# Kernel tuning notes

Hardware: AMD Instinct MI355X
Metric: run time of the kernel (lower is better)

Reference implementation:

```python
import jax, jax.numpy as jnp
import numpy as np

NUM_CLASSES = 8
EPS = 1e-4  # variance epsilon from the original module
MARGIN = 1.0  # __init__ arg; unused in the forward math


def setup_inputs() -> dict:
    key = jax.random.key(0)
    kf, kl = jax.random.split(key)
    features = jax.random.normal(kf, (65536, 2, 256), dtype=jnp.float32)
    labels = jax.random.randint(kl, (65536,), 0, NUM_CLASSES)
    return {"features": features, "labels": labels}


def _loss(features, labels):
    B, V, D = features.shape
    # Views of each sample are stacked into the sample's class group
    X = features.reshape(B * V, D)              # [N, D]
    lab = jnp.repeat(labels, V)                 # [N]
    onehot = (lab[:, None] == jnp.arange(NUM_CLASSES)[None, :]).astype(X.dtype)  # [N, C]

    counts = onehot.sum(axis=0)                 # [C] per-class row counts (all > 1 by construction)
    sums = onehot.T @ X                         # [C, D]
    means = sums / counts[:, None]              # [C, D]
    e2 = onehot.T @ (X * X)                     # [C, D] per-class sum of squares
    # unbiased per-feature variance (torch.var default, ddof=1)
    var = (e2 - counts[:, None] * means * means) / (counts[:, None] - 1.0)
    std = jnp.sqrt(var + EPS)
    std_loss = jnp.sum(jnp.mean(jax.nn.relu(1.0 - std), axis=1))  # sum over classes of mean over features

    # Per-class covariance: cov_c = (X_c - mu_c)^T (X_c - mu_c) / (n_c - 1)
    #                             = (sum_c x x^T - n_c mu mu^T) / (n_c - 1)
    S = jnp.einsum('nc,nd,ne->cde', onehot, X, X)  # [C, D, D]
    cov = (S - counts[:, None, None] * means[:, :, None] * means[:, None, :]) / (
        counts[:, None, None] - 1.0)
    diag = jnp.diagonal(cov, axis1=1, axis2=2)      # [C, D]
    offdiag_sq = jnp.sum(cov * cov, axis=(1, 2)) - jnp.sum(diag * diag, axis=1)
    cov_loss = jnp.sum(offdiag_sq / D)

    return std_loss + cov_loss


def reference(features, labels):
    return _loss(features, labels)
```

## Files before the change

kernel.cpp:

```cpp
#include <hip/hip_runtime.h>
#include <stdint.h>


#define NCLS  8
#define D     256
#define CHUNK 512
#define SEG   256
#define EPSF  1e-4f
#define TMAX  264
#define QLEN  16384

typedef __bf16 bf16x8 __attribute__((ext_vector_type(8)));
typedef float  f32x4  __attribute__((ext_vector_type(4)));

__device__ __forceinline__ unsigned short f2bf(float f) {
    unsigned int x = __float_as_uint(f);
    x += 0x7fffu + ((x >> 16) & 1u);
    return (unsigned short)(x >> 16);
}
__device__ __forceinline__ float bf2f(unsigned short u) {
    return __uint_as_float(((unsigned int)u) << 16);
}
__device__ __forceinline__ uint4 pack8(const f32x4& a, const f32x4& b) {
    return make_uint4(
        (unsigned int)f2bf(a[0]) | ((unsigned int)f2bf(a[1]) << 16),
        (unsigned int)f2bf(a[2]) | ((unsigned int)f2bf(a[3]) << 16),
        (unsigned int)f2bf(b[0]) | ((unsigned int)f2bf(b[1]) << 16),
        (unsigned int)f2bf(b[2]) | ((unsigned int)f2bf(b[3]) << 16));
}
__device__ __forceinline__ void st_tile(unsigned char* lds, const uint4* R,
                                        int kblk, int cblkg) {
    #pragma unroll
    for (int cc = 0; cc < 8; ++cc) {
        int wd = cc >> 1;
        int sh = (cc & 1) * 16;
        unsigned int e0 = (((const unsigned int*)&R[0])[wd] >> sh) & 0xffffu;
        unsigned int e1 = (((const unsigned int*)&R[1])[wd] >> sh) & 0xffffu;
        unsigned int e2 = (((const unsigned int*)&R[2])[wd] >> sh) & 0xffffu;
        unsigned int e3 = (((const unsigned int*)&R[3])[wd] >> sh) & 0xffffu;
        int ccol = cblkg * 8 + cc;
        int byt = ccol * 128 + ((kblk * 8) ^ (cc << 4));
        *(uint2*)(lds + byt) = make_uint2(e0 | (e1 << 16), e2 | (e3 << 16));
    }
}

__global__ void k_hist(const int* __restrict__ labels, int nlab, int vfac,
                       int* __restrict__ counts) {
    __shared__ int lc[NCLS];
    int t = threadIdx.x;
    if (t < NCLS) lc[t] = 0;
    __syncthreads();
    for (int i = blockIdx.x * blockDim.x + t; i < nlab; i += gridDim.x * blockDim.x)
        atomicAdd(&lc[labels[i] & 7], vfac);
    __syncthreads();
    if (t < NCLS && lc[t]) atomicAdd(&counts[t], lc[t]);
}

__global__ void k_offsets(const int* __restrict__ counts,
                          int* __restrict__ offsets, int* __restrict__ cursor) {
    if (threadIdx.x == 0) {
        int acc = 0;
        for (int c = 0; c < NCLS; ++c) { offsets[c] = acc; cursor[c] = acc; acc += counts[c]; }
    }
}

__global__ __launch_bounds__(256) void k_idx(
    const int* __restrict__ labels, int nrows, int vfac,
    int* __restrict__ cursor, int* __restrict__ idx)
{
    __shared__ int lcnt[NCLS], lbase[NCLS];
    int t = threadIdx.x;
    int row = blockIdx.x * SEG + t;
    if (t < NCLS) lcnt[t] = 0;
    __syncthreads();
    int c = 0, rk = 0;
    bool ok = (row < nrows);
    if (ok) {
        c = labels[row / vfac] & 7;
        rk = atomicAdd(&lcnt[c], 1);
    }
    __syncthreads();
    if (t < NCLS) lbase[t] = lcnt[t] ? atomicAdd(&cursor[t], lcnt[t]) : 0;
    __syncthreads();
    if (ok) idx[lbase[c] + rk] = row;
}

__global__ __launch_bounds__(256) void k_gram_g(
    const float* __restrict__ X, const int* __restrict__ idx,
    const int* __restrict__ counts, const int* __restrict__ offsets,
    unsigned short* __restrict__ part, float* __restrict__ csums)
{
    __shared__ __align__(16) unsigned char lds[64 * 256 * 2];

    int t = threadIdx.x;
    int lane = t & 63;
    int w = t >> 6;
    int wrow = w >> 1, wcol = w & 1;
    int kblk = t & 15;
    int cblk0 = t >> 4;

    int nch[NCLS], ofch[NCLS];
    int T = 0;
    for (int c = 0; c < NCLS; ++c) {
        int n = counts[c];
        nch[c] = (n + CHUNK - 1) / CHUNK;
        ofch[c] = T;
        T += nch[c];
    }

    const f32x4 zf = {0.f, 0.f, 0.f, 0.f};

    for (int wk = blockIdx.x; wk < 3 * T; wk += gridDim.x) {
        int item = wk / 3;
        int q = wk - item * 3;
        int c = 0;
        while (c < NCLS - 1 && item >= ofch[c + 1]) ++c;
        int chunk = item - ofch[c];
        int base = offsets[c] + chunk * CHUNK;
        int rows = min(CHUNK, counts[c] - chunk * CHUNK);
        int ntiles = (rows + 63) >> 6;

        int colb = (q == 1) ? 128 : 0;
        bool two = (q == 2);
        int bbase = two ? 128 : 0;

        f32x4 acc[4][4];
        #pragma unroll
        for (int i = 0; i < 4; ++i)
            #pragma unroll
            for (int j = 0; j < 4; ++j)
                #pragma unroll
                for (int r = 0; r < 4; ++r) acc[i][j][r] = 0.f;
        float sumv[8];
        #pragma unroll
        for (int e = 0; e < 8; ++e) sumv[e] = 0.f;

        for (int kt = 0; kt < ntiles; ++kt) {
            int rid[4];
            #pragma unroll
            for (int j = 0; j < 4; ++j) {
                int r = kt * 64 + kblk * 4 + j;
                rid[j] = idx[base + min(r, rows - 1)];
            }
            uint4 R0[4];
            #pragma unroll
            for (int j = 0; j < 4; ++j) {
                int r = kt * 64 + kblk * 4 + j;
                const float* rp = X + ((size_t)rid[j] << 8) + colb + cblk0 * 8;
                f32x4 a = *(const f32x4*)rp;
                f32x4 b = *(const f32x4*)(rp + 4);
                if (r >= rows) { a = zf; b = zf; }
                #pragma unroll
                for (int e = 0; e < 4; ++e) { sumv[e] += a[e]; sumv[4 + e] += b[e]; }
                R0[j] = pack8(a, b);
            }
            uint4 R1[4];
            if (two) {
                #pragma unroll
                for (int j = 0; j < 4; ++j) {
                    int r = kt * 64 + kblk * 4 + j;
                    const float* rp = X + ((size_t)rid[j] << 8) + 128 + cblk0 * 8;
                    f32x4 a = *(const f32x4*)rp;
                    f32x4 b = *(const f32x4*)(rp + 4);
                    if (r >= rows) { a = zf; b = zf; }
                    R1[j] = pack8(a, b);
                }
            }
            __syncthreads();
            st_tile(lds, R0, kblk, cblk0);
            if (two) st_tile(lds, R1, kblk, cblk0 + 16);
            __syncthreads();
            #pragma unroll
            for (int ks = 0; ks < 2; ++ks) {
                int kb2 = ks * 64 + ((lane >> 4) << 4);
                int swz = (lane & 7) << 4;
                bf16x8 bfr[4];
                #pragma unroll
                for (int tj = 0; tj < 4; ++tj) {
                    int ccol = bbase + wcol * 64 + tj * 16 + (lane & 15);
                    bfr[tj] = __builtin_bit_cast(bf16x8,
                        *(const uint4*)(lds + ccol * 128 + (kb2 ^ swz)));
                }
                #pragma unroll
                for (int ti = 0; ti < 4; ++ti) {
                    int ccol = wrow * 64 + ti * 16 + (lane & 15);
                    bf16x8 af = __builtin_bit_cast(bf16x8,
                        *(const uint4*)(lds + ccol * 128 + (kb2 ^ swz)));
                    #pragma unroll
                    for (int tj = 0; tj < 4; ++tj)
                        acc[ti][tj] = __builtin_amdgcn_mfma_f32_16x16x32_bf16(
                            af, bfr[tj], acc[ti][tj], 0, 0, 0);
                }
            }
        }

        unsigned short* dst = part + (size_t)wk * QLEN;
        #pragma unroll
        for (int ti = 0; ti < 4; ++ti) {
            int row0 = wrow * 64 + ti * 16 + ((lane >> 4) << 2);
            #pragma unroll
            for (int tj = 0; tj < 4; ++tj) {
                int col = wcol * 64 + tj * 16 + (lane & 15);
                #pragma unroll
                for (int r = 0; r < 4; ++r)
                    dst[(row0 + r) * 128 + col] = f2bf(acc[ti][tj][r]);
            }
        }

        #pragma unroll
        for (int s = 1; s < 16; s <<= 1)
            #pragma unroll
            for (int e = 0; e < 8; ++e)
                sumv[e] += __shfl_xor(sumv[e], s, 64);
        if (q < 2 && (t & 15) == 0) {
            float* cs = csums + (size_t)item * D + colb + cblk0 * 8;
            #pragma unroll
            for (int e = 0; e < 8; ++e) cs[e] = sumv[e];
        }
        __syncthreads();
    }
}

__global__ __launch_bounds__(256) void k_gsum(
    const float* __restrict__ csums, const int* __restrict__ counts,
    float* __restrict__ gsums)
{
    int c = blockIdx.x;
    int i = threadIdx.x;
    int of = 0;
    for (int cc = 0; cc < c; ++cc) of += (counts[cc] + CHUNK - 1) / CHUNK;
    int nc = (counts[c] + CHUNK - 1) / CHUNK;
    float s = 0.f;
    for (int q = 0; q < nc; ++q) s += csums[(size_t)(of + q) * D + i];
    gsums[c * D + i] = s;
}

__global__ __launch_bounds__(256) void k_loss(
    const unsigned short* __restrict__ part, const float* __restrict__ gsums,
    const int* __restrict__ counts, float* __restrict__ out)
{
    __shared__ float red[256];
    int t = threadIdx.x;
    int nch[NCLS], ofch[NCLS];
    int T = 0;
    for (int c = 0; c < NCLS; ++c) {
        int n = counts[c];
        nch[c] = (n + CHUNK - 1) / CHUNK;
        ofch[c] = T;
        T += nch[c];
    }
    float local = 0.f;
    const int total = NCLS * 3 * QLEN;
    for (int idx = blockIdx.x * blockDim.x + t; idx < total; idx += gridDim.x * blockDim.x) {
        int c = idx / (3 * QLEN);
        int rem = idx - c * (3 * QLEN);
        int q = rem >> 14;
        int ij = rem & (QLEN - 1);
        int il = ij >> 7, jl = ij & 127;
        int gi = il + ((q == 1) ? 128 : 0);
        int gj = jl + ((q == 0) ? 0 : 128);
        const unsigned short* p = part + ((size_t)(ofch[c] * 3 + q)) * QLEN + ij;
        float s = 0.f;
        for (int k = 0; k < nch[c]; ++k) s += bf2f(p[(size_t)k * 3 * QLEN]);
        float n  = (float)counts[c];
        float mi = gsums[c * D + gi] / n;
        float mj = gsums[c * D + gj] / n;
        float cov = (s - n * mi * mj) / (n - 1.f);
        float contrib;
        if (q == 2) {
            contrib = 2.f * cov * cov * (1.f / (float)D);
        } else if (il == jl) {
            float sd = sqrtf(cov + EPSF);
            contrib = fmaxf(1.f - sd, 0.f) * (1.f / (float)D);
        } else {
            contrib = cov * cov * (1.f / (float)D);
        }
        local += contrib;
    }
    red[t] = local;
    __syncthreads();
    for (int s = 128; s > 0; s >>= 1) {
        if (t < s) red[t] += red[t + s];
        __syncthreads();
    }
    if (t == 0) atomicAdd(out, red[0]);
}

extern "C" void kernel_launch(void* const* d_in, const int* in_sizes, int n_in,
                              void* d_out, int out_size, void* d_ws, size_t ws_size,
                              hipStream_t stream)
{
    const float* X      = (const float*)d_in[0];
    const int*   labels = (const int*)d_in[1];
    int nfeat = in_sizes[0];
    int nlab  = in_sizes[1];
    int nrows = nfeat / D;
    int vfac  = nrows / nlab;

    char* ws = (char*)d_ws;
    size_t off_idx   = 0;
    size_t sz_idx    = (size_t)nrows * 4;
    size_t off_part  = (off_idx + sz_idx + 255) & ~(size_t)255;
    size_t sz_part   = (size_t)3 * TMAX * QLEN * 2;
    size_t off_cs    = (off_part + sz_part + 255) & ~(size_t)255;
    size_t sz_cs     = (size_t)TMAX * D * 4;
    size_t off_gs    = (off_cs + sz_cs + 255) & ~(size_t)255;
    size_t sz_gs     = (size_t)NCLS * D * 4;
    size_t off_cnt   = (off_gs + sz_gs + 255) & ~(size_t)255;
    size_t off_ofs   = off_cnt + 64;
    size_t off_cur   = off_ofs + 64;

    int*            idx     = (int*)(ws + off_idx);
    unsigned short* part    = (unsigned short*)(ws + off_part);
    float*          csums   = (float*)(ws + off_cs);
    float*          gsums   = (float*)(ws + off_gs);
    int*            counts  = (int*)(ws + off_cnt);
    int*            offsets = (int*)(ws + off_ofs);
    int*            cursor  = (int*)(ws + off_cur);

    hipMemsetAsync(counts, 0, 64, stream);
    hipMemsetAsync(d_out, 0, (size_t)out_size * sizeof(float), stream);

    k_hist<<<64, 256, 0, stream>>>(labels, nlab, vfac, counts);
    k_offsets<<<1, 64, 0, stream>>>(counts, offsets, cursor);
    k_idx<<<(nrows + SEG - 1) / SEG, SEG, 0, stream>>>(labels, nrows, vfac, cursor, idx);
    k_gram_g<<<3 * TMAX, 256, 0, stream>>>(X, idx, counts, offsets, part, csums);
    k_gsum<<<NCLS, 256, 0, stream>>>(csums, counts, gsums);
    k_loss<<<512, 256, 0, stream>>>(part, gsums, counts, (float*)d_out);
}
```

Before: 134.6 us.

## Pre-transpose sorted rows to bf16 and run Gram with per-class split-K partials

Adds a transpose kernel that gathers class-sorted rows, converts them to bf16 in a feature-major per-chunk layout and computes column sums. A new Gram kernel then reads MFMA fragments straight from global memory with no LDS staging, splitting each class's chunks across G groups so the partial buffer shrinks to 8*3*G tiles. The loss kernel reduces over G instead of per-chunk partials. It adds an extra pass writing roughly 64MB of bf16 and depends on workspace size to pick the path, falling back to the old pipeline otherwise; the idx buffer aliases the partial slab, which is only safe because idx is consumed before the Gram kernel writes.

```diff
diff --git a/kernel.cpp b/kernel.cpp
--- a/kernel.cpp
+++ b/kernel.cpp
@@ -7,7 +7,8 @@
 #define CHUNK 512
 #define SEG   256
 #define EPSF  1e-4f
-#define TMAX  264
+#define TCMAX 263
+#define TMAXF 264
 #define QLEN  16384
 
 typedef __bf16 bf16x8 __attribute__((ext_vector_type(8)));
@@ -21,6 +22,242 @@
 __device__ __forceinline__ float bf2f(unsigned short u) {
     return __uint_as_float(((unsigned int)u) << 16);
 }
+
+__global__ void k_hist(const int* __restrict__ labels, int nlab, int vfac,
+                       int* __restrict__ counts) {
+    __shared__ int lc[NCLS];
+    int t = threadIdx.x;
+    if (t < NCLS) lc[t] = 0;
+    __syncthreads();
+    for (int i = blockIdx.x * blockDim.x + t; i < nlab; i += gridDim.x * blockDim.x)
+        atomicAdd(&lc[labels[i] & 7], vfac);
+    __syncthreads();
+    if (t < NCLS && lc[t]) atomicAdd(&counts[t], lc[t]);
+}
+
+__global__ void k_offsets(const int* __restrict__ counts,
+                          int* __restrict__ offsets, int* __restrict__ cursor) {
+    if (threadIdx.x == 0) {
+        int acc = 0;
+        for (int c = 0; c < NCLS; ++c) { offsets[c] = acc; cursor[c] = acc; acc += counts[c]; }
+    }
+}
+
+__global__ __launch_bounds__(256) void k_idx(
+    const int* __restrict__ labels, int nrows, int vfac,
+    int* __restrict__ cursor, int* __restrict__ idx)
+{
+    __shared__ int lcnt[NCLS], lbase[NCLS];
+    int t = threadIdx.x;
+    int row = blockIdx.x * SEG + t;
+    if (t < NCLS) lcnt[t] = 0;
+    __syncthreads();
+    int c = 0, rk = 0;
+    bool ok = (row < nrows);
+    if (ok) {
+        c = labels[row / vfac] & 7;
+        rk = atomicAdd(&lcnt[c], 1);
+    }
+    __syncthreads();
+    if (t < NCLS) lbase[t] = lcnt[t] ? atomicAdd(&cursor[t], lcnt[t]) : 0;
+    __syncthreads();
+    if (ok) idx[lbase[c] + rk] = row;
+}
+
+__global__ __launch_bounds__(512) void k_tr(
+    const float* __restrict__ X, const int* __restrict__ idx,
+    const int* __restrict__ counts, const int* __restrict__ offsets,
+    unsigned short* __restrict__ sortedT, float* __restrict__ csums)
+{
+    int t = threadIdx.x;
+    int fg = t >> 5, rg = t & 31;
+
+    int nch[NCLS], ofch[NCLS];
+    int T = 0;
+    for (int c = 0; c < NCLS; ++c) {
+        nch[c] = (counts[c] + CHUNK - 1) / CHUNK;
+        ofch[c] = T;
+        T += nch[c];
+    }
+    const f32x4 zf = {0.f, 0.f, 0.f, 0.f};
+
+    for (int wk = blockIdx.x; wk < 2 * T; wk += gridDim.x) {
+        int ch = wk >> 1, ph = wk & 1;
+        int c = 0;
+        while (c < NCLS - 1 && ch >= ofch[c + 1]) ++c;
+        int m = ch - ofch[c];
+        int base = offsets[c] + m * CHUNK;
+        int rows = min(CHUNK, counts[c] - m * CHUNK);
+        unsigned short* out = sortedT + ((size_t)ch << 17);
+
+        for (int p = ph * 2; p < ph * 2 + 2; ++p) {
+            float s0 = 0.f, s1 = 0.f, s2 = 0.f, s3 = 0.f;
+            for (int it = 0; it < 4; ++it) {
+                int r0 = it * 128 + rg * 4;
+                f32x4 v[4];
+                #pragma unroll
+                for (int j = 0; j < 4; ++j) {
+                    int r = r0 + j;
+                    int rid = idx[base + min(r, rows - 1)];
+                    f32x4 x = *(const f32x4*)(X + ((size_t)rid << 8) + p * 64 + fg * 4);
+                    if (r >= rows) x = zf;
+                    v[j] = x;
+                }
+                s0 += v[0][0] + v[1][0] + v[2][0] + v[3][0];
+                s1 += v[0][1] + v[1][1] + v[2][1] + v[3][1];
+                s2 += v[0][2] + v[1][2] + v[2][2] + v[3][2];
+                s3 += v[0][3] + v[1][3] + v[2][3] + v[3][3];
+                #pragma unroll
+                for (int e = 0; e < 4; ++e) {
+                    unsigned int b0 = (unsigned int)f2bf(v[0][e]) | ((unsigned int)f2bf(v[1][e]) << 16);
+                    unsigned int b1 = (unsigned int)f2bf(v[2][e]) | ((unsigned int)f2bf(v[3][e]) << 16);
+                    int f = p * 64 + fg * 4 + e;
+                    *(uint2*)(out + (size_t)f * CHUNK + r0) = make_uint2(b0, b1);
+                }
+            }
+            #pragma unroll
+            for (int sh = 1; sh < 32; sh <<= 1) {
+                s0 += __shfl_xor(s0, sh, 64);
+                s1 += __shfl_xor(s1, sh, 64);
+                s2 += __shfl_xor(s2, sh, 64);
+                s3 += __shfl_xor(s3, sh, 64);
+            }
+            if (rg == 0) {
+                f32x4 sv = {s0, s1, s2, s3};
+                *(f32x4*)(csums + (size_t)ch * D + p * 64 + fg * 4) = sv;
+            }
+        }
+    }
+}
+
+__global__ __launch_bounds__(256) void k_gram_s(
+    const unsigned short* __restrict__ sortedT, const int* __restrict__ counts,
+    unsigned short* __restrict__ part, int G)
+{
+    int t = threadIdx.x;
+    int lane = t & 63;
+    int w = t >> 6;
+    int wr = w >> 1, wc = w & 1;
+
+    int wk = blockIdx.x;
+    int c = wk / (3 * G);
+    int rem = wk - c * (3 * G);
+    int q = rem / G;
+    int g = rem - q * G;
+
+    int och = 0;
+    for (int cc = 0; cc < c; ++cc) och += (counts[cc] + CHUNK - 1) / CHUNK;
+    int nchc = (counts[c] + CHUNK - 1) / CHUNK;
+
+    int rowb = (q == 1) ? 128 : 0;
+    int colb = (q == 0) ? 0 : 128;
+    int fr_a = rowb + wr * 64 + (lane & 15);
+    int fr_b = colb + wc * 64 + (lane & 15);
+    int kh = (lane >> 4) * 8;
+
+    f32x4 acc[4][4];
+    #pragma unroll
+    for (int i = 0; i < 4; ++i)
+        #pragma unroll
+        for (int j = 0; j < 4; ++j)
+            #pragma unroll
+            for (int r = 0; r < 4; ++r) acc[i][j][r] = 0.f;
+
+    for (int m = g; m < nchc; m += G) {
+        const unsigned short* cb = sortedT + ((size_t)(och + m) << 17);
+        const unsigned short* pa = cb + (size_t)fr_a * CHUNK + kh;
+        const unsigned short* pb = cb + (size_t)fr_b * CHUNK + kh;
+        for (int ks = 0; ks < CHUNK / 32; ++ks) {
+            int ke = ks * 32;
+            bf16x8 afr[4], bfr[4];
+            #pragma unroll
+            for (int ti = 0; ti < 4; ++ti)
+                afr[ti] = __builtin_bit_cast(bf16x8,
+                    *(const uint4*)(pa + (size_t)ti * 16 * CHUNK + ke));
+            #pragma unroll
+            for (int tj = 0; tj < 4; ++tj)
+                bfr[tj] = __builtin_bit_cast(bf16x8,
+                    *(const uint4*)(pb + (size_t)tj * 16 * CHUNK + ke));
+            #pragma unroll
+            for (int ti = 0; ti < 4; ++ti)
+                #pragma unroll
+                for (int tj = 0; tj < 4; ++tj)
+                    acc[ti][tj] = __builtin_amdgcn_mfma_f32_16x16x32_bf16(
+                        afr[ti], bfr[tj], acc[ti][tj], 0, 0, 0);
+        }
+    }
+
+    unsigned short* dst = part + (size_t)wk * QLEN;
+    #pragma unroll
+    for (int ti = 0; ti < 4; ++ti) {
+        int row0 = wr * 64 + ti * 16 + ((lane >> 4) << 2);
+        #pragma unroll
+        for (int tj = 0; tj < 4; ++tj) {
+            int col = wc * 64 + tj * 16 + (lane & 15);
+            #pragma unroll
+            for (int r = 0; r < 4; ++r)
+                dst[(row0 + r) * 128 + col] = f2bf(acc[ti][tj][r]);
+        }
+    }
+}
+
+__global__ __launch_bounds__(256) void k_gsum(
+    const float* __restrict__ csums, const int* __restrict__ counts,
+    float* __restrict__ gsums)
+{
+    int c = blockIdx.x;
+    int i = threadIdx.x;
+    int of = 0;
+    for (int cc = 0; cc < c; ++cc) of += (counts[cc] + CHUNK - 1) / CHUNK;
+    int nc = (counts[c] + CHUNK - 1) / CHUNK;
+    float s = 0.f;
+    for (int q = 0; q < nc; ++q) s += csums[(size_t)(of + q) * D + i];
+    gsums[c * D + i] = s;
+}
+
+__global__ __launch_bounds__(256) void k_loss_s(
+    const unsigned short* __restrict__ part, const float* __restrict__ gsums,
+    const int* __restrict__ counts, float* __restrict__ out, int G)
+{
+    __shared__ float red[256];
+    int t = threadIdx.x;
+    float local = 0.f;
+    const int total = NCLS * 3 * QLEN;
+    for (int idx = blockIdx.x * blockDim.x + t; idx < total; idx += gridDim.x * blockDim.x) {
+        int c = idx / (3 * QLEN);
+        int rem = idx - c * (3 * QLEN);
+        int q = rem >> 14;
+        int ij = rem & (QLEN - 1);
+        int il = ij >> 7, jl = ij & 127;
+        int gi = il + ((q == 1) ? 128 : 0);
+        int gj = jl + ((q == 0) ? 0 : 128);
+        const unsigned short* p = part + ((size_t)((c * 3 + q) * G)) * QLEN + ij;
+        float s = 0.f;
+        for (int g = 0; g < G; ++g) s += bf2f(p[(size_t)g * QLEN]);
+        float n  = (float)counts[c];
+        float mi = gsums[c * D + gi] / n;
+        float mj = gsums[c * D + gj] / n;
+        float cov = (s - n * mi * mj) / (n - 1.f);
+        float contrib;
+        if (q == 2) {
+            contrib = 2.f * cov * cov * (1.f / (float)D);
+        } else if (il == jl) {
+            float sd = sqrtf(cov + EPSF);
+            contrib = fmaxf(1.f - sd, 0.f) * (1.f / (float)D);
+        } else {
+            contrib = cov * cov * (1.f / (float)D);
+        }
+        local += contrib;
+    }
+    red[t] = local;
+    __syncthreads();
+    for (int s = 128; s > 0; s >>= 1) {
+        if (t < s) red[t] += red[t + s];
+        __syncthreads();
+    }
+    if (t == 0) atomicAdd(out, red[0]);
+}
+
 __device__ __forceinline__ uint4 pack8(const f32x4& a, const f32x4& b) {
     return make_uint4(
         (unsigned int)f2bf(a[0]) | ((unsigned int)f2bf(a[1]) << 16),
@@ -44,54 +281,12 @@
     }
 }
 
-__global__ void k_hist(const int* __restrict__ labels, int nlab, int vfac,
-                       int* __restrict__ counts) {
-    __shared__ int lc[NCLS];
-    int t = threadIdx.x;
-    if (t < NCLS) lc[t] = 0;
-    __syncthreads();
-    for (int i = blockIdx.x * blockDim.x + t; i < nlab; i += gridDim.x * blockDim.x)
-        atomicAdd(&lc[labels[i] & 7], vfac);
-    __syncthreads();
-    if (t < NCLS && lc[t]) atomicAdd(&counts[t], lc[t]);
-}
-
-__global__ void k_offsets(const int* __restrict__ counts,
-                          int* __restrict__ offsets, int* __restrict__ cursor) {
-    if (threadIdx.x == 0) {
-        int acc = 0;
-        for (int c = 0; c < NCLS; ++c) { offsets[c] = acc; cursor[c] = acc; acc += counts[c]; }
-    }
-}
-
-__global__ __launch_bounds__(256) void k_idx(
-    const int* __restrict__ labels, int nrows, int vfac,
-    int* __restrict__ cursor, int* __restrict__ idx)
-{
-    __shared__ int lcnt[NCLS], lbase[NCLS];
-    int t = threadIdx.x;
-    int row = blockIdx.x * SEG + t;
-    if (t < NCLS) lcnt[t] = 0;
-    __syncthreads();
-    int c = 0, rk = 0;
-    bool ok = (row < nrows);
-    if (ok) {
-        c = labels[row / vfac] & 7;
-        rk = atomicAdd(&lcnt[c], 1);
-    }
-    __syncthreads();
-    if (t < NCLS) lbase[t] = lcnt[t] ? atomicAdd(&cursor[t], lcnt[t]) : 0;
-    __syncthreads();
-    if (ok) idx[lbase[c] + rk] = row;
-}
-
-__global__ __launch_bounds__(256) void k_gram_g(
+__global__ __launch_bounds__(256) void k_gram_f(
     const float* __restrict__ X, const int* __restrict__ idx,
     const int* __restrict__ counts, const int* __restrict__ offsets,
     unsigned short* __restrict__ part, float* __restrict__ csums)
 {
     __shared__ __align__(16) unsigned char lds[64 * 256 * 2];
-
     int t = threadIdx.x;
     int lane = t & 63;
     int w = t >> 6;
@@ -102,12 +297,10 @@
     int nch[NCLS], ofch[NCLS];
     int T = 0;
     for (int c = 0; c < NCLS; ++c) {
-        int n = counts[c];
-        nch[c] = (n + CHUNK - 1) / CHUNK;
+        nch[c] = (counts[c] + CHUNK - 1) / CHUNK;
         ofch[c] = T;
         T += nch[c];
     }
-
     const f32x4 zf = {0.f, 0.f, 0.f, 0.f};
 
     for (int wk = blockIdx.x; wk < 3 * T; wk += gridDim.x) {
@@ -120,7 +313,7 @@
         int rows = min(CHUNK, counts[c] - chunk * CHUNK);
         int ntiles = (rows + 63) >> 6;
 
-        int colb = (q == 1) ? 128 : 0;
+        int colbg = (q == 1) ? 128 : 0;
         bool two = (q == 2);
         int bbase = two ? 128 : 0;
 
@@ -146,7 +339,7 @@
             #pragma unroll
             for (int j = 0; j < 4; ++j) {
                 int r = kt * 64 + kblk * 4 + j;
-                const float* rp = X + ((size_t)rid[j] << 8) + colb + cblk0 * 8;
+                const float* rp = X + ((size_t)rid[j] << 8) + colbg + cblk0 * 8;
                 f32x4 a = *(const f32x4*)rp;
                 f32x4 b = *(const f32x4*)(rp + 4);
                 if (r >= rows) { a = zf; b = zf; }
@@ -206,14 +399,13 @@
                     dst[(row0 + r) * 128 + col] = f2bf(acc[ti][tj][r]);
             }
         }
-
         #pragma unroll
         for (int s = 1; s < 16; s <<= 1)
             #pragma unroll
             for (int e = 0; e < 8; ++e)
                 sumv[e] += __shfl_xor(sumv[e], s, 64);
         if (q < 2 && (t & 15) == 0) {
-            float* cs = csums + (size_t)item * D + colb + cblk0 * 8;
+            float* cs = csums + (size_t)item * D + colbg + cblk0 * 8;
             #pragma unroll
             for (int e = 0; e < 8; ++e) cs[e] = sumv[e];
         }
@@ -221,21 +413,7 @@
     }
 }
 
-__global__ __launch_bounds__(256) void k_gsum(
-    const float* __restrict__ csums, const int* __restrict__ counts,
-    float* __restrict__ gsums)
-{
-    int c = blockIdx.x;
-    int i = threadIdx.x;
-    int of = 0;
-    for (int cc = 0; cc < c; ++cc) of += (counts[cc] + CHUNK - 1) / CHUNK;
-    int nc = (counts[c] + CHUNK - 1) / CHUNK;
-    float s = 0.f;
-    for (int q = 0; q < nc; ++q) s += csums[(size_t)(of + q) * D + i];
-    gsums[c * D + i] = s;
-}
-
-__global__ __launch_bounds__(256) void k_loss(
+__global__ __launch_bounds__(256) void k_loss_f(
     const unsigned short* __restrict__ part, const float* __restrict__ gsums,
     const int* __restrict__ counts, float* __restrict__ out)
 {
@@ -244,8 +422,7 @@
     int nch[NCLS], ofch[NCLS];
     int T = 0;
     for (int c = 0; c < NCLS; ++c) {
-        int n = counts[c];
-        nch[c] = (n + CHUNK - 1) / CHUNK;
+        nch[c] = (counts[c] + CHUNK - 1) / CHUNK;
         ofch[c] = T;
         T += nch[c];
     }
@@ -298,33 +475,72 @@
     int vfac  = nrows / nlab;
 
     char* ws = (char*)d_ws;
-    size_t off_idx   = 0;
-    size_t sz_idx    = (size_t)nrows * 4;
-    size_t off_part  = (off_idx + sz_idx + 255) & ~(size_t)255;
-    size_t sz_part   = (size_t)3 * TMAX * QLEN * 2;
-    size_t off_cs    = (off_part + sz_part + 255) & ~(size_t)255;
-    size_t sz_cs     = (size_t)TMAX * D * 4;
-    size_t off_gs    = (off_cs + sz_cs + 255) & ~(size_t)255;
-    size_t sz_gs     = (size_t)NCLS * D * 4;
-    size_t off_cnt   = (off_gs + sz_gs + 255) & ~(size_t)255;
-    size_t off_ofs   = off_cnt + 64;
-    size_t off_cur   = off_ofs + 64;
-
-    int*            idx     = (int*)(ws + off_idx);
-    unsigned short* part    = (unsigned short*)(ws + off_part);
-    float*          csums   = (float*)(ws + off_cs);
-    float*          gsums   = (float*)(ws + off_gs);
-    int*            counts  = (int*)(ws + off_cnt);
-    int*            offsets = (int*)(ws + off_ofs);
-    int*            cursor  = (int*)(ws + off_cur);
-
-    hipMemsetAsync(counts, 0, 64, stream);
-    hipMemsetAsync(d_out, 0, (size_t)out_size * sizeof(float), stream);
-
-    k_hist<<<64, 256, 0, stream>>>(labels, nlab, vfac, counts);
-    k_offsets<<<1, 64, 0, stream>>>(counts, offsets, cursor);
-    k_idx<<<(nrows + SEG - 1) / SEG, SEG, 0, stream>>>(labels, nrows, vfac, cursor, idx);
-    k_gram_g<<<3 * TMAX, 256, 0, stream>>>(X, idx, counts, offsets, part, csums);
-    k_gsum<<<NCLS, 256, 0, stream>>>(csums, counts, gsums);
-    k_loss<<<512, 256, 0, stream>>>(part, gsums, counts, (float*)d_out);
-}
+
+    size_t sz_sT    = (size_t)TCMAX * CHUNK * D * 2;
+    size_t off_cs   = sz_sT;
+    size_t sz_cs    = (size_t)TCMAX * D * 4;
+    size_t off_cnt  = (off_cs + sz_cs + 255) & ~(size_t)255;
+    size_t off_ofs  = off_cnt + 64;
+    size_t off_cur  = off_ofs + 64;
+    size_t off_slab = (off_cur + 64 + 255) & ~(size_t)255;
+    size_t unit     = (size_t)NCLS * 3 * QLEN * 2;
+
+    int G = 0;
+    if (ws_size > off_slab + 4096) G = (int)((ws_size - off_slab - 4096) / unit);
+    if (G > 32) G = 32;
+
+    if (G >= 12) {
+        unsigned short* sortedT = (unsigned short*)(ws);
+        float*          csums   = (float*)(ws + off_cs);
+        int*            counts  = (int*)(ws + off_cnt);
+        int*            offsets = (int*)(ws + off_ofs);
+        int*            cursor  = (int*)(ws + off_cur);
+        unsigned short* part    = (unsigned short*)(ws + off_slab);
+        int*            idx     = (int*)(ws + off_slab);
+        float*          gsums   = (float*)(ws + off_cnt + 256);
+        gsums = (float*)(ws + off_cur + 64);
+        gsums = csums + (size_t)TCMAX * D;
+        gsums = (float*)(ws + off_slab + (size_t)G * unit);
+
+        hipMemsetAsync(counts, 0, 64, stream);
+        hipMemsetAsync(d_out, 0, (size_t)out_size * sizeof(float), stream);
+
+        k_hist<<<64, 256, 0, stream>>>(labels, nlab, vfac, counts);
+        k_offsets<<<1, 64, 0, stream>>>(counts, offsets, cursor);
+        k_idx<<<(nrows + SEG - 1) / SEG, SEG, 0, stream>>>(labels, nrows, vfac, cursor, idx);
+        k_tr<<<2 * TCMAX, 512, 0, stream>>>(X, idx, counts, offsets, sortedT, csums);
+        k_gram_s<<<NCLS * 3 * G, 256, 0, stream>>>(sortedT, counts, part, G);
+        k_gsum<<<NCLS, 256, 0, stream>>>(csums, counts, gsums);
+        k_loss_s<<<512, 256, 0, stream>>>(part, gsums, counts, (float*)d_out, G);
+    } else {
+        size_t off_idx  = 0;
+        size_t sz_idx   = (size_t)nrows * 4;
+        size_t off_part = (off_idx + sz_idx + 255) & ~(size_t)255;
+        size_t sz_part  = (size_t)3 * TMAXF * QLEN * 2;
+        size_t off_cs2  = (off_part + sz_part + 255) & ~(size_t)255;
+        size_t sz_cs2   = (size_t)TMAXF * D * 4;
+        size_t off_gs   = (off_cs2 + sz_cs2 + 255) & ~(size_t)255;
+        size_t sz_gs    = (size_t)NCLS * D * 4;
+        size_t off_cn2  = (off_gs + sz_gs + 255) & ~(size_t)255;
+        size_t off_of2  = off_cn2 + 64;
+        size_t off_cu2  = off_of2 + 64;
+
+        int*            idx     = (int*)(ws + off_idx);
+        unsigned short* part    = (unsigned short*)(ws + off_part);
+        float*          csums   = (float*)(ws + off_cs2);
+        float*          gsums   = (float*)(ws + off_gs);
+        int*            counts  = (int*)(ws + off_cn2);
+        int*            offsets = (int*)(ws + off_of2);
+        int*            cursor  = (int*)(ws + off_cu2);
+
+        hipMemsetAsync(counts, 0, 64, stream);
+        hipMemsetAsync(d_out, 0, (size_t)out_size * sizeof(float), stream);
+
+        k_hist<<<64, 256, 0, stream>>>(labels, nlab, vfac, counts);
+        k_offsets<<<1, 64, 0, stream>>>(counts, offsets, cursor);
+        k_idx<<<(nrows + SEG - 1) / SEG, SEG, 0, stream>>>(labels, nrows, vfac, cursor, idx);
+        k_gram_f<<<3 * TMAXF, 256, 0, stream>>>(X, idx, counts, offsets, part, csums);
+        k_gsum<<<NCLS, 256, 0, stream>>>(csums, counts, gsums);
+        k_loss_f<<<512, 256, 0, stream>>>(part, gsums, counts, (float*)d_out);
+    }
+}
```

New measurement: 187.0 us. 1.39x slower.

## Scatter features into class-sorted bf16 buffer before Gram accumulation

Applied to the files above, without the earlier changes.

Adds a scatter pass that converts X to bf16 and writes rows into a class-contiguous sorted buffer while accumulating per-class column sums. The Gram kernel then reads contiguous bf16 rows instead of gathering fp32 rows through an index array. It also uses a fixed grid of class×quadrant×G blocks that loop over chunks, with 512-thread blocks and smaller per-wave tiles, and drops the separate gsum kernel. In exchange it adds an extra full read of X plus a bf16 write and reread, and G depends on workspace size.

```diff
diff --git a/kernel.cpp b/kernel.cpp
--- a/kernel.cpp
+++ b/kernel.cpp
@@ -4,10 +4,9 @@
 
 #define NCLS  8
 #define D     256
-#define CHUNK 512
+#define CHUNK 1024
 #define SEG   256
 #define EPSF  1e-4f
-#define TMAX  264
 #define QLEN  16384
 
 typedef __bf16 bf16x8 __attribute__((ext_vector_type(8)));
@@ -20,13 +19,6 @@
 }
 __device__ __forceinline__ float bf2f(unsigned short u) {
     return __uint_as_float(((unsigned int)u) << 16);
-}
-__device__ __forceinline__ uint4 pack8(const f32x4& a, const f32x4& b) {
-    return make_uint4(
-        (unsigned int)f2bf(a[0]) | ((unsigned int)f2bf(a[1]) << 16),
-        (unsigned int)f2bf(a[2]) | ((unsigned int)f2bf(a[3]) << 16),
-        (unsigned int)f2bf(b[0]) | ((unsigned int)f2bf(b[1]) << 16),
-        (unsigned int)f2bf(b[2]) | ((unsigned int)f2bf(b[3]) << 16));
 }
 __device__ __forceinline__ void st_tile(unsigned char* lds, const uint4* R,
                                         int kblk, int cblkg) {
@@ -64,9 +56,9 @@
     }
 }
 
-__global__ __launch_bounds__(256) void k_idx(
+__global__ __launch_bounds__(256) void k_rank(
     const int* __restrict__ labels, int nrows, int vfac,
-    int* __restrict__ cursor, int* __restrict__ idx)
+    int* __restrict__ cursor, int* __restrict__ rank)
 {
     __shared__ int lcnt[NCLS], lbase[NCLS];
     int t = threadIdx.x;
@@ -82,173 +74,161 @@
     __syncthreads();
     if (t < NCLS) lbase[t] = lcnt[t] ? atomicAdd(&cursor[t], lcnt[t]) : 0;
     __syncthreads();
-    if (ok) idx[lbase[c] + rk] = row;
-}
-
-__global__ __launch_bounds__(256) void k_gram_g(
-    const float* __restrict__ X, const int* __restrict__ idx,
+    if (ok) rank[row] = lbase[c] + rk;
+}
+
+__global__ __launch_bounds__(512) void k_scatter(
+    const float* __restrict__ X, const int* __restrict__ labels,
+    const int* __restrict__ rank, int nrows, int vfac,
+    unsigned short* __restrict__ sorted, float* __restrict__ gsums)
+{
+    __shared__ float sumbuf[8][NCLS][4][64];
+    int t = threadIdx.x;
+    int w = t >> 6, lane = t & 63;
+
+    for (int i = t; i < 8 * NCLS * 4 * 64; i += 512)
+        (&sumbuf[0][0][0][0])[i] = 0.f;
+    __syncthreads();
+
+    int r0w = blockIdx.x * 512 + w * 64;
+    if (r0w < nrows) {
+        int myrow = r0w + lane;
+        int rankv = (myrow < nrows) ? rank[myrow] : 0;
+        int labv  = (myrow < nrows) ? (labels[myrow / vfac] & 7) : 0;
+        int nloc = min(64, nrows - r0w);
+        for (int i = 0; i < nloc; ++i) {
+            int dest = __shfl(rankv, i, 64);
+            int c    = __shfl(labv, i, 64);
+            f32x4 v = *(const f32x4*)(X + ((size_t)(r0w + i) << 8) + lane * 4);
+            float* sc = &sumbuf[w][c][0][lane];
+            sc[0]   += v[0];
+            sc[64]  += v[1];
+            sc[128] += v[2];
+            sc[192] += v[3];
+            ushort4 o;
+            o.x = f2bf(v[0]); o.y = f2bf(v[1]); o.z = f2bf(v[2]); o.w = f2bf(v[3]);
+            *(ushort4*)(sorted + ((size_t)dest << 8) + lane * 4) = o;
+        }
+    }
+    __syncthreads();
+
+    for (int s = t; s < NCLS * 4 * 64; s += 512) {
+        float val = 0.f;
+        #pragma unroll
+        for (int wb = 0; wb < 8; ++wb)
+            val += (&sumbuf[0][0][0][0])[wb * (NCLS * 4 * 64) + s];
+        if (val != 0.f) {
+            int c  = s >> 8;
+            int e  = (s >> 6) & 3;
+            int ln = s & 63;
+            atomicAdd(&gsums[c * D + ln * 4 + e], val);
+        }
+    }
+}
+
+__global__ __launch_bounds__(512) void k_gram(
+    const unsigned short* __restrict__ sorted,
     const int* __restrict__ counts, const int* __restrict__ offsets,
-    unsigned short* __restrict__ part, float* __restrict__ csums)
+    unsigned short* __restrict__ part, int G)
 {
     __shared__ __align__(16) unsigned char lds[64 * 256 * 2];
 
     int t = threadIdx.x;
     int lane = t & 63;
     int w = t >> 6;
-    int wrow = w >> 1, wcol = w & 1;
+    int wr = w >> 2, wc = w & 3;
     int kblk = t & 15;
     int cblk0 = t >> 4;
 
-    int nch[NCLS], ofch[NCLS];
-    int T = 0;
-    for (int c = 0; c < NCLS; ++c) {
-        int n = counts[c];
-        nch[c] = (n + CHUNK - 1) / CHUNK;
-        ofch[c] = T;
-        T += nch[c];
-    }
-
-    const f32x4 zf = {0.f, 0.f, 0.f, 0.f};
-
-    for (int wk = blockIdx.x; wk < 3 * T; wk += gridDim.x) {
-        int item = wk / 3;
-        int q = wk - item * 3;
-        int c = 0;
-        while (c < NCLS - 1 && item >= ofch[c + 1]) ++c;
-        int chunk = item - ofch[c];
-        int base = offsets[c] + chunk * CHUNK;
-        int rows = min(CHUNK, counts[c] - chunk * CHUNK);
+    int blk = blockIdx.x;
+    int c = blk / (3 * G);
+    int rem = blk - c * (3 * G);
+    int q = rem / G;
+    int g = rem - q * G;
+
+    int base0 = offsets[c];
+    int n = counts[c];
+    int nch = (n + CHUNK - 1) / CHUNK;
+
+    int np   = (q == 2) ? 32 : 16;
+    int colb = (q == 1) ? 128 : 0;
+    int bbase = (q == 2) ? 128 : 0;
+
+    f32x4 acc[4][2];
+    #pragma unroll
+    for (int i = 0; i < 4; ++i)
+        #pragma unroll
+        for (int j = 0; j < 2; ++j)
+            #pragma unroll
+            for (int r = 0; r < 4; ++r) acc[i][j][r] = 0.f;
+
+    bool st = (cblk0 < np);
+    const uint4 zq = make_uint4(0u, 0u, 0u, 0u);
+
+    for (int m = g; m < nch; m += G) {
+        int base = base0 + m * CHUNK;
+        int rows = min(CHUNK, n - m * CHUNK);
         int ntiles = (rows + 63) >> 6;
-
-        int colb = (q == 1) ? 128 : 0;
-        bool two = (q == 2);
-        int bbase = two ? 128 : 0;
-
-        f32x4 acc[4][4];
-        #pragma unroll
-        for (int i = 0; i < 4; ++i)
-            #pragma unroll
-            for (int j = 0; j < 4; ++j)
-                #pragma unroll
-                for (int r = 0; r < 4; ++r) acc[i][j][r] = 0.f;
-        float sumv[8];
-        #pragma unroll
-        for (int e = 0; e < 8; ++e) sumv[e] = 0.f;
-
         for (int kt = 0; kt < ntiles; ++kt) {
-            int rid[4];
-            #pragma unroll
-            for (int j = 0; j < 4; ++j) {
-                int r = kt * 64 + kblk * 4 + j;
-                rid[j] = idx[base + min(r, rows - 1)];
-            }
-            uint4 R0[4];
-            #pragma unroll
-            for (int j = 0; j < 4; ++j) {
-                int r = kt * 64 + kblk * 4 + j;
-                const float* rp = X + ((size_t)rid[j] << 8) + colb + cblk0 * 8;
-                f32x4 a = *(const f32x4*)rp;
-                f32x4 b = *(const f32x4*)(rp + 4);
-                if (r >= rows) { a = zf; b = zf; }
-                #pragma unroll
-                for (int e = 0; e < 4; ++e) { sumv[e] += a[e]; sumv[4 + e] += b[e]; }
-                R0[j] = pack8(a, b);
-            }
-            uint4 R1[4];
-            if (two) {
+            uint4 R[4];
+            if (st) {
                 #pragma unroll
                 for (int j = 0; j < 4; ++j) {
                     int r = kt * 64 + kblk * 4 + j;
-                    const float* rp = X + ((size_t)rid[j] << 8) + 128 + cblk0 * 8;
-                    f32x4 a = *(const f32x4*)rp;
-                    f32x4 b = *(const f32x4*)(rp + 4);
-                    if (r >= rows) { a = zf; b = zf; }
-                    R1[j] = pack8(a, b);
+                    R[j] = (r < rows)
+                        ? *(const uint4*)(sorted + (((size_t)(base + r)) << 8)
+                                          + colb + cblk0 * 8)
+                        : zq;
                 }
             }
             __syncthreads();
-            st_tile(lds, R0, kblk, cblk0);
-            if (two) st_tile(lds, R1, kblk, cblk0 + 16);
+            if (st) st_tile(lds, R, kblk, cblk0);
             __syncthreads();
             #pragma unroll
             for (int ks = 0; ks < 2; ++ks) {
                 int kb2 = ks * 64 + ((lane >> 4) << 4);
                 int swz = (lane & 7) << 4;
-                bf16x8 bfr[4];
+                bf16x8 bfr[2];
                 #pragma unroll
-                for (int tj = 0; tj < 4; ++tj) {
-                    int ccol = bbase + wcol * 64 + tj * 16 + (lane & 15);
+                for (int tj = 0; tj < 2; ++tj) {
+                    int ccol = bbase + wc * 32 + tj * 16 + (lane & 15);
                     bfr[tj] = __builtin_bit_cast(bf16x8,
                         *(const uint4*)(lds + ccol * 128 + (kb2 ^ swz)));
                 }
                 #pragma unroll
                 for (int ti = 0; ti < 4; ++ti) {
-                    int ccol = wrow * 64 + ti * 16 + (lane & 15);
+                    int ccol = wr * 64 + ti * 16 + (lane & 15);
                     bf16x8 af = __builtin_bit_cast(bf16x8,
                         *(const uint4*)(lds + ccol * 128 + (kb2 ^ swz)));
                     #pragma unroll
-                    for (int tj = 0; tj < 4; ++tj)
+                    for (int tj = 0; tj < 2; ++tj)
                         acc[ti][tj] = __builtin_amdgcn_mfma_f32_16x16x32_bf16(
                             af, bfr[tj], acc[ti][tj], 0, 0, 0);
                 }
             }
         }
-
-        unsigned short* dst = part + (size_t)wk * QLEN;
+    }
+
+    unsigned short* dst = part + (size_t)blk * QLEN;
+    #pragma unroll
+    for (int ti = 0; ti < 4; ++ti) {
+        int row0 = wr * 64 + ti * 16 + ((lane >> 4) << 2);
         #pragma unroll
-        for (int ti = 0; ti < 4; ++ti) {
-            int row0 = wrow * 64 + ti * 16 + ((lane >> 4) << 2);
+        for (int tj = 0; tj < 2; ++tj) {
+            int col = wc * 32 + tj * 16 + (lane & 15);
             #pragma unroll
-            for (int tj = 0; tj < 4; ++tj) {
-                int col = wcol * 64 + tj * 16 + (lane & 15);
-                #pragma unroll
-                for (int r = 0; r < 4; ++r)
-                    dst[(row0 + r) * 128 + col] = f2bf(acc[ti][tj][r]);
-            }
-        }
-
-        #pragma unroll
-        for (int s = 1; s < 16; s <<= 1)
-            #pragma unroll
-            for (int e = 0; e < 8; ++e)
-                sumv[e] += __shfl_xor(sumv[e], s, 64);
-        if (q < 2 && (t & 15) == 0) {
-            float* cs = csums + (size_t)item * D + colb + cblk0 * 8;
-            #pragma unroll
-            for (int e = 0; e < 8; ++e) cs[e] = sumv[e];
-        }
-        __syncthreads();
-    }
-}
-
-__global__ __launch_bounds__(256) void k_gsum(
-    const float* __restrict__ csums, const int* __restrict__ counts,
-    float* __restrict__ gsums)
-{
-    int c = blockIdx.x;
-    int i = threadIdx.x;
-    int of = 0;
-    for (int cc = 0; cc < c; ++cc) of += (counts[cc] + CHUNK - 1) / CHUNK;
-    int nc = (counts[c] + CHUNK - 1) / CHUNK;
-    float s = 0.f;
-    for (int q = 0; q < nc; ++q) s += csums[(size_t)(of + q) * D + i];
-    gsums[c * D + i] = s;
+            for (int r = 0; r < 4; ++r)
+                dst[(row0 + r) * 128 + col] = f2bf(acc[ti][tj][r]);
+        }
+    }
 }
 
 __global__ __launch_bounds__(256) void k_loss(
     const unsigned short* __restrict__ part, const float* __restrict__ gsums,
-    const int* __restrict__ counts, float* __restrict__ out)
+    const int* __restrict__ counts, float* __restrict__ out, int G)
 {
     __shared__ float red[256];
     int t = threadIdx.x;
-    int nch[NCLS], ofch[NCLS];
-    int T = 0;
-    for (int c = 0; c < NCLS; ++c) {
-        int n = counts[c];
-        nch[c] = (n + CHUNK - 1) / CHUNK;
-        ofch[c] = T;
-        T += nch[c];
-    }
     float local = 0.f;
     const int total = NCLS * 3 * QLEN;
     for (int idx = blockIdx.x * blockDim.x + t; idx < total; idx += gridDim.x * blockDim.x) {
@@ -259,9 +239,9 @@
         int il = ij >> 7, jl = ij & 127;
         int gi = il + ((q == 1) ? 128 : 0);
         int gj = jl + ((q == 0) ? 0 : 128);
-        const unsigned short* p = part + ((size_t)(ofch[c] * 3 + q)) * QLEN + ij;
+        const unsigned short* p = part + ((size_t)((c * 3 + q) * G)) * QLEN + ij;
         float s = 0.f;
-        for (int k = 0; k < nch[c]; ++k) s += bf2f(p[(size_t)k * 3 * QLEN]);
+        for (int g = 0; g < G; ++g) s += bf2f(p[(size_t)g * QLEN]);
         float n  = (float)counts[c];
         float mi = gsums[c * D + gi] / n;
         float mj = gsums[c * D + gj] / n;
@@ -298,33 +278,40 @@
     int vfac  = nrows / nlab;
 
     char* ws = (char*)d_ws;
-    size_t off_idx   = 0;
-    size_t sz_idx    = (size_t)nrows * 4;
-    size_t off_part  = (off_idx + sz_idx + 255) & ~(size_t)255;
-    size_t sz_part   = (size_t)3 * TMAX * QLEN * 2;
-    size_t off_cs    = (off_part + sz_part + 255) & ~(size_t)255;
-    size_t sz_cs     = (size_t)TMAX * D * 4;
-    size_t off_gs    = (off_cs + sz_cs + 255) & ~(size_t)255;
-    size_t sz_gs     = (size_t)NCLS * D * 4;
-    size_t off_cnt   = (off_gs + sz_gs + 255) & ~(size_t)255;
-    size_t off_ofs   = off_cnt + 64;
-    size_t off_cur   = off_ofs + 64;
-
-    int*            idx     = (int*)(ws + off_idx);
-    unsigned short* part    = (unsigned short*)(ws + off_part);
-    float*          csums   = (float*)(ws + off_cs);
+    size_t off_sorted = 0;
+    size_t sz_sorted  = (size_t)nrows * D * 2;
+    size_t off_rank   = (off_sorted + sz_sorted + 255) & ~(size_t)255;
+    size_t sz_rank    = (size_t)nrows * 4;
+    size_t off_gs     = (off_rank + sz_rank + 255) & ~(size_t)255;
+    size_t sz_gs      = (size_t)NCLS * D * 4;
+    size_t off_cnt    = (off_gs + sz_gs + 255) & ~(size_t)255;
+    size_t off_ofs    = off_cnt + 64;
+    size_t off_cur    = off_ofs + 64;
+    size_t off_part   = (off_cur + 64 + 255) & ~(size_t)255;
+
+    size_t slab_bytes = (size_t)QLEN * 2;
+    long long avail = (long long)ws_size - (long long)off_part;
+    int G = (int)(avail / (long long)(3 * NCLS * slab_bytes));
+    if (G > 32) G = 32;
+    if (G < 1)  G = 1;
+
+    unsigned short* sorted  = (unsigned short*)(ws + off_sorted);
+    int*            rank    = (int*)(ws + off_rank);
     float*          gsums   = (float*)(ws + off_gs);
     int*            counts  = (int*)(ws + off_cnt);
     int*            offsets = (int*)(ws + off_ofs);
     int*            cursor  = (int*)(ws + off_cur);
+    unsigned short* part    = (unsigned short*)(ws + off_part);
 
     hipMemsetAsync(counts, 0, 64, stream);
+    hipMemsetAsync(gsums, 0, sz_gs, stream);
     hipMemsetAsync(d_out, 0, (size_t)out_size * sizeof(float), stream);
 
     k_hist<<<64, 256, 0, stream>>>(labels, nlab, vfac, counts);
     k_offsets<<<1, 64, 0, stream>>>(counts, offsets, cursor);
-    k_idx<<<(nrows + SEG - 1) / SEG, SEG, 0, stream>>>(labels, nrows, vfac, cursor, idx);
-    k_gram_g<<<3 * TMAX, 256, 0, stream>>>(X, idx, counts, offsets, part, csums);
-    k_gsum<<<NCLS, 256, 0, stream>>>(csums, counts, gsums);
-    k_loss<<<512, 256, 0, stream>>>(part, gsums, counts, (float*)d_out);
-}
+    k_rank<<<(nrows + SEG - 1) / SEG, SEG, 0, stream>>>(labels, nrows, vfac, cursor, rank);
+    k_scatter<<<(nrows + 511) / 512, 512, 0, stream>>>(
+        X, labels, rank, nrows, vfac, sorted, gsums);
+    k_gram<<<NCLS * 3 * G, 512, 0, stream>>>(sorted, counts, offsets, part, G);
+    k_loss<<<512, 256, 0, stream>>>(part, gsums, counts, (float*)d_out, G);
+}
```

New measurement: 308.1 us. +129.0%, slower.
